# Performance work log

Hardware: AMD Instinct MI355X
Metric: run time of the kernel (lower is better)

## Reference

```python
import jax, jax.numpy as jnp
import numpy as np

EPS = 1e-8           # torch F.cosine_similarity eps
GLOBAL_COEFF = 0.5   # config.global_coeff


def setup_inputs() -> dict:
    key = jax.random.key(0)
    k1, k2, k3 = jax.random.split(key, 3)
    B, P, D = 8192, 1024, 2048
    return {
        "ppg": jax.random.normal(k1, (B, 1, D), dtype=jnp.float32),
        "keys": jax.random.normal(k2, (P, D), dtype=jnp.float32),
        "prompt": jax.random.normal(k3, (P, D), dtype=jnp.float32),
        "k": 5,
    }


def reference(ppg, keys, prompt, k):
    # ppg: [B,1,D], keys/prompt: [P,D]
    q = ppg[:, 0, :]                                   # [B,D]
    dot = jnp.einsum('bd,pd->bp', q, keys)             # [B,P]
    qn = jnp.linalg.norm(q, axis=-1, keepdims=True)    # [B,1]
    kn = jnp.linalg.norm(keys, axis=-1)[None, :]       # [1,P]
    cos = dot / jnp.maximum(qn * kn, EPS)
    score_ = 1.0 - cos                                 # [B,P]

    # top-k smallest distances
    neg_vals, idx = jax.lax.top_k(-score_, k)          # idx: [B,k]
    sel_score = -neg_vals                              # [B,k]

    # softmax over pool, global entropy (summed over batch AND pool, as in torch code)
    logp = jax.nn.log_softmax(score_, axis=-1)
    probs = jnp.exp(logp)
    entropy = -jnp.sum(probs * logp)

    # masked prompt aggregation == sum of the k selected prompts per batch element
    # (original builds a [B,P,D] mask; gather is the same math without the blowup)
    sel_prompts = prompt[idx]                          # [B,k,D]
    agg = sel_prompts.sum(axis=1)[:, None, :]          # [B,1,D]

    prompted = ppg + GLOBAL_COEFF * agg                # [B,1,D]
    # score.sum() in torch: (score_ * topk_mask).sum() == sel_score.sum()
    return prompted, sel_score.sum(), entropy
```

## Files before the change

### kernel.cpp

```cpp
#include <hip/hip_runtime.h>
#include <stdint.h>

#define NB 8192
#define NP 1024
#define ND 2048
#define KSEL 5

typedef unsigned short u16;
typedef unsigned int u32;
typedef unsigned long long u64;
typedef __attribute__((ext_vector_type(8))) short bf16x8;
typedef __attribute__((ext_vector_type(8))) u16 u16x8;
typedef __attribute__((ext_vector_type(4))) u16 u16x4;
typedef __attribute__((ext_vector_type(4))) float f32x4;

__device__ float g_knf[NP];
__device__ float g_qn[NB];
__device__ float g_psel[NB];
__device__ float g_pent[NB];
__device__ int   g_cidx[NB * 8];

__device__ __forceinline__ u16 f2bf_rne(float f) {
    u32 u = __float_as_uint(f);
    u = (u + 0x7fffu + ((u >> 16) & 1u)) >> 16;
    return (u16)u;
}


__global__ __launch_bounds__(256) void prep_q(const float* __restrict__ q,
                                              u16* __restrict__ qb) {
    const int r = blockIdx.x, t = threadIdx.x;
    const float* row = q + (size_t)r * ND;
    float4 a = *(const float4*)(row + t * 8);
    float4 b = *(const float4*)(row + t * 8 + 4);
    if (qb) {
        u16x8 v;
        v[0] = f2bf_rne(a.x); v[1] = f2bf_rne(a.y); v[2] = f2bf_rne(a.z); v[3] = f2bf_rne(a.w);
        v[4] = f2bf_rne(b.x); v[5] = f2bf_rne(b.y); v[6] = f2bf_rne(b.z); v[7] = f2bf_rne(b.w);
        *(u16x8*)(qb + (size_t)r * ND + t * 8) = v;
    }
    float ss = a.x*a.x + a.y*a.y + a.z*a.z + a.w*a.w
             + b.x*b.x + b.y*b.y + b.z*b.z + b.w*b.w;
    for (int off = 32; off; off >>= 1) ss += __shfl_xor(ss, off);
    __shared__ float red[4];
    if ((t & 63) == 0) red[t >> 6] = ss;
    __syncthreads();
    if (t == 0) g_qn[r] = sqrtf(red[0] + red[1] + red[2] + red[3]);
}

__global__ __launch_bounds__(256) void prep_k(const float* __restrict__ k,
                                              u16* __restrict__ kb) {
    const int r = blockIdx.x, t = threadIdx.x;
    const float* row = k + (size_t)r * ND;
    float4 a = *(const float4*)(row + t * 8);
    float4 b = *(const float4*)(row + t * 8 + 4);
    if (kb) {
        u16x8 v;
        v[0] = f2bf_rne(a.x); v[1] = f2bf_rne(a.y); v[2] = f2bf_rne(a.z); v[3] = f2bf_rne(a.w);
        v[4] = f2bf_rne(b.x); v[5] = f2bf_rne(b.y); v[6] = f2bf_rne(b.z); v[7] = f2bf_rne(b.w);
        *(u16x8*)(kb + (size_t)r * ND + t * 8) = v;
    }
    float ss = a.x*a.x + a.y*a.y + a.z*a.z + a.w*a.w
             + b.x*b.x + b.y*b.y + b.z*b.z + b.w*b.w;
    for (int off = 32; off; off >>= 1) ss += __shfl_xor(ss, off);
    __shared__ float red[4];
    if ((t & 63) == 0) red[t >> 6] = ss;
    __syncthreads();
    if (t == 0) g_knf[r] = sqrtf(red[0] + red[1] + red[2] + red[3]);
}


__global__ __launch_bounds__(256) void gemm_fast(const u16* __restrict__ A,
                                                 const u16* __restrict__ B,
                                                 float* __restrict__ C) {
    __shared__ u16 As[128 * 64];
    __shared__ u16 Bs[128 * 64];
    const int t = threadIdx.x, w = t >> 6, l = t & 63;
    const int bid = blockIdx.x;
    const int m0 = (bid >> 3) << 7, n0 = (bid & 7) << 7;
    const int wr = w >> 1, wc = w & 1;

    f32x4 acc[4][4];
#pragma unroll
    for (int m = 0; m < 4; m++)
#pragma unroll
        for (int n = 0; n < 4; n++) acc[m][n] = (f32x4){0.f, 0.f, 0.f, 0.f};

    const int rowi = l >> 3, col8 = l & 7;
    const u16* Abase = A + (size_t)(m0 + w * 8 + rowi) * ND + col8 * 8;
    const u16* Bbase = B + (size_t)(n0 + w * 8 + rowi) * ND + col8 * 8;

    for (int k0 = 0; k0 < ND; k0 += 64) {
#pragma unroll
        for (int i = 0; i < 4; i++) {
            __builtin_amdgcn_global_load_lds(
                (const __attribute__((address_space(1))) void*)(Abase + (size_t)(i * 32) * ND + k0),
                (__attribute__((address_space(3))) void*)(&As[(i * 4 + w) * 512]),
                16, 0, 0);
            __builtin_amdgcn_global_load_lds(
                (const __attribute__((address_space(1))) void*)(Bbase + (size_t)(i * 32) * ND + k0),
                (__attribute__((address_space(3))) void*)(&Bs[(i * 4 + w) * 512]),
                16, 0, 0);
        }
        __syncthreads();
#pragma unroll
        for (int kk = 0; kk < 64; kk += 32) {
            bf16x8 af[4], bfr[4];
#pragma unroll
            for (int m = 0; m < 4; m++)
                af[m] = *(const bf16x8*)&As[(wr * 64 + m * 16 + (l & 15)) * 64 + kk + (l >> 4) * 8];
#pragma unroll
            for (int n = 0; n < 4; n++)
                bfr[n] = *(const bf16x8*)&Bs[(wc * 64 + n * 16 + (l & 15)) * 64 + kk + (l >> 4) * 8];
#pragma unroll
            for (int m = 0; m < 4; m++)
#pragma unroll
                for (int n = 0; n < 4; n++)
                    acc[m][n] = __builtin_amdgcn_mfma_f32_16x16x32_bf16(af[m], bfr[n], acc[m][n], 0, 0, 0);
        }
        __syncthreads();
    }

    const int lc = l & 15, lr4 = (l >> 4) * 4;
#pragma unroll
    for (int m = 0; m < 4; m++) {
        int rbase = m0 + wr * 64 + m * 16 + lr4;
#pragma unroll
        for (int n = 0; n < 4; n++) {
            int col = n0 + wc * 64 + n * 16 + lc;
#pragma unroll
            for (int r = 0; r < 4; r++)
                C[(size_t)(rbase + r) * NP + col] = acc[m][n][r];
        }
    }
}


__global__ __launch_bounds__(256) void gemm_slow(const float* __restrict__ A,
                                                 const float* __restrict__ B,
                                                 float* __restrict__ C) {
    __shared__ u16 As[128 * 64];
    __shared__ u16 Bs[128 * 64];
    const int t = threadIdx.x, w = t >> 6, l = t & 63;
    const int bid = blockIdx.x;
    const int m0 = (bid >> 3) << 7, n0 = (bid & 7) << 7;
    const int wr = w >> 1, wc = w & 1;

    f32x4 acc[4][4];
#pragma unroll
    for (int m = 0; m < 4; m++)
#pragma unroll
        for (int n = 0; n < 4; n++) acc[m][n] = (f32x4){0.f, 0.f, 0.f, 0.f};

    const int arow = t >> 4;
    const int acol4 = t & 15;

    for (int k0 = 0; k0 < ND; k0 += 64) {
#pragma unroll
        for (int s = 0; s < 8; s++) {
            int row = s * 16 + arow;
            float4 va = *(const float4*)(A + (size_t)(m0 + row) * ND + k0 + acol4 * 4);
            u16x4 ba;
            ba[0] = f2bf_rne(va.x); ba[1] = f2bf_rne(va.y);
            ba[2] = f2bf_rne(va.z); ba[3] = f2bf_rne(va.w);
            *(u16x4*)&As[row * 64 + acol4 * 4] = ba;
            float4 vb = *(const float4*)(B + (size_t)(n0 + row) * ND + k0 + acol4 * 4);
            u16x4 bb;
            bb[0] = f2bf_rne(vb.x); bb[1] = f2bf_rne(vb.y);
            bb[2] = f2bf_rne(vb.z); bb[3] = f2bf_rne(vb.w);
            *(u16x4*)&Bs[row * 64 + acol4 * 4] = bb;
        }
        __syncthreads();
#pragma unroll
        for (int kk = 0; kk < 64; kk += 32) {
            bf16x8 af[4], bfr[4];
#pragma unroll
            for (int m = 0; m < 4; m++)
                af[m] = *(const bf16x8*)&As[(wr * 64 + m * 16 + (l & 15)) * 64 + kk + (l >> 4) * 8];
#pragma unroll
            for (int n = 0; n < 4; n++)
                bfr[n] = *(const bf16x8*)&Bs[(wc * 64 + n * 16 + (l & 15)) * 64 + kk + (l >> 4) * 8];
#pragma unroll
            for (int m = 0; m < 4; m++)
#pragma unroll
                for (int n = 0; n < 4; n++)
                    acc[m][n] = __builtin_amdgcn_mfma_f32_16x16x32_bf16(af[m], bfr[n], acc[m][n], 0, 0, 0);
        }
        __syncthreads();
    }

    const int lc = l & 15, lr4 = (l >> 4) * 4;
#pragma unroll
    for (int m = 0; m < 4; m++) {
        int rbase = m0 + wr * 64 + m * 16 + lr4;
#pragma unroll
        for (int n = 0; n < 4; n++) {
            int col = n0 + wc * 64 + n * 16 + lc;
#pragma unroll
            for (int r = 0; r < 4; r++)
                C[(size_t)(rbase + r) * NP + col] = acc[m][n][r];
        }
    }
}


__global__ __launch_bounds__(256) void rowstats(const float* __restrict__ C) {
    const int l = threadIdx.x & 63;
    const int r = blockIdx.x * 4 + (threadIdx.x >> 6);
    const float qn = g_qn[r];

    const float* crow = C + (size_t)r * NP;
    float s[16];
#pragma unroll
    for (int j = 0; j < 16; j++) {
        float dot = crow[j * 64 + l];
        float kn = g_knf[j * 64 + l];
        s[j] = 1.0f - dot / fmaxf(qn * kn, 1e-8f);
    }

    float mx = s[0];
#pragma unroll
    for (int j = 1; j < 16; j++) mx = fmaxf(mx, s[j]);
    for (int off = 32; off; off >>= 1) mx = fmaxf(mx, __shfl_xor(mx, off));
    float S0 = 0.f, S1 = 0.f;
#pragma unroll
    for (int j = 0; j < 16; j++) {
        float d = s[j] - mx;
        float e = __expf(d);
        S0 += e;
        S1 += d * e;
    }
    for (int off = 32; off; off >>= 1) {
        S0 += __shfl_xor(S0, off);
        S1 += __shfl_xor(S1, off);
    }

    unsigned used = 0;
    float ssum = 0.f;
    int ci[KSEL];
    for (int i = 0; i < KSEL; i++) {
        float bv = 3.0e38f;
        int bp = 0;
#pragma unroll
        for (int j = 0; j < 16; j++) {
            if (!((used >> j) & 1) && s[j] < bv) { bv = s[j]; bp = j * 64 + l; }
        }
        u64 u = ((u64)__float_as_uint(bv) << 32) | (u32)bp;
        for (int off = 32; off; off >>= 1) {
            u64 o = __shfl_xor(u, off);
            if (o < u) u = o;
        }
        int p = (int)(u & 0xffffffffu);
        ci[i] = p;
        ssum += __uint_as_float((u32)(u >> 32));
        if ((p & 63) == l) used |= 1u << (p >> 6);
    }
    if (l == 0) {
        g_pent[r] = logf(S0) - S1 / S0;
        g_psel[r] = ssum;
#pragma unroll
        for (int i = 0; i < KSEL; i++) g_cidx[r * 8 + i] = ci[i];
    }
}


__global__ __launch_bounds__(256) void gather_out(const float* __restrict__ ppg,
                                                  const float* __restrict__ prompt,
                                                  float* __restrict__ outp) {
    const int r = blockIdx.x, t = threadIdx.x;
    __shared__ int sel[KSEL];
    if (t < KSEL) sel[t] = g_cidx[r * 8 + t];
    __syncthreads();

    const float* prow = ppg + (size_t)r * ND + t * 8;
    float4 a = *(const float4*)prow;
    float4 b = *(const float4*)(prow + 4);
    float4 ax = {0, 0, 0, 0}, bx = {0, 0, 0, 0};
#pragma unroll
    for (int i = 0; i < KSEL; i++) {
        const float* pr = prompt + (size_t)sel[i] * ND + t * 8;
        float4 x = *(const float4*)pr;
        float4 y = *(const float4*)(pr + 4);
        ax.x += x.x; ax.y += x.y; ax.z += x.z; ax.w += x.w;
        bx.x += y.x; bx.y += y.y; bx.z += y.z; bx.w += y.w;
    }
    float4 oa = {a.x + 0.5f * ax.x, a.y + 0.5f * ax.y, a.z + 0.5f * ax.z, a.w + 0.5f * ax.w};
    float4 ob = {b.x + 0.5f * bx.x, b.y + 0.5f * bx.y, b.z + 0.5f * bx.z, b.w + 0.5f * bx.w};
    float* orow = outp + (size_t)r * ND + t * 8;
    *(float4*)orow = oa;
    *(float4*)(orow + 4) = ob;
}


__global__ __launch_bounds__(1024) void finalize_scal(float* __restrict__ outp) {
    const int t = threadIdx.x;
    float a = 0.f, b = 0.f;
#pragma unroll
    for (int i = 0; i < NB / 1024; i++) {
        a += g_psel[i * 1024 + t];
        b += g_pent[i * 1024 + t];
    }
    for (int off = 32; off; off >>= 1) {
        a += __shfl_xor(a, off);
        b += __shfl_xor(b, off);
    }
    __shared__ float ra[16], rb[16];
    if ((t & 63) == 0) { ra[t >> 6] = a; rb[t >> 6] = b; }
    __syncthreads();
    if (t == 0) {
        float sa = 0.f, sb = 0.f;
#pragma unroll
        for (int i = 0; i < 16; i++) { sa += ra[i]; sb += rb[i]; }
        outp[(size_t)NB * ND] = sa;
        outp[(size_t)NB * ND + 1] = sb;
    }
}

extern "C" void kernel_launch(void* const* d_in, const int* in_sizes, int n_in,
                              void* d_out, int out_size, void* d_ws, size_t ws_size,
                              hipStream_t stream) {
    const float* ppg    = (const float*)d_in[0];
    const float* keys   = (const float*)d_in[1];
    const float* prompt = (const float*)d_in[2];
    float* outp = (float*)d_out;

    float* C = (float*)d_out;

    const size_t QB_BYTES = (size_t)NB * ND * 2;
    const size_t KB_BYTES = (size_t)NP * ND * 2;
    bool fast = (d_ws != nullptr) && (ws_size >= QB_BYTES + KB_BYTES);
    u16* qb = fast ? (u16*)d_ws : nullptr;
    u16* kb = fast ? (u16*)((char*)d_ws + QB_BYTES) : nullptr;

    prep_q<<<NB, 256, 0, stream>>>(ppg, qb);
    prep_k<<<NP, 256, 0, stream>>>(keys, kb);
    if (fast) {
        gemm_fast<<<(NB / 128) * (NP / 128), 256, 0, stream>>>(qb, kb, C);
    } else {
        gemm_slow<<<(NB / 128) * (NP / 128), 256, 0, stream>>>(ppg, keys, C);
    }
    rowstats<<<NB / 4, 256, 0, stream>>>(C);
    gather_out<<<NB, 256, 0, stream>>>(ppg, prompt, outp);
    finalize_scal<<<1, 1024, 0, stream>>>(outp);
}
```

Measured before the change: 245.9 us.

## Fuse cosine epilogue into GEMM, store bf16 scores, merge rowstats with gather

The query and key prep kernels become one launch. The GEMM now runs 512 threads per block with a two-row-group load layout and an XCD-aware tile mapping, and its epilogue applies the cosine normalization and stores scores as bf16 into a global buffer. A single post kernel then computes the row softmax entropy, top-k and prompt gather-sum, which removes the fp32 score round-trip and the index buffer between kernels. Rounding scores to bf16 before top-k and entropy can reorder close candidates and shift the entropy.

```diff
diff --git a/kernel.cpp b/kernel.cpp
--- a/kernel.cpp
+++ b/kernel.cpp
@@ -18,26 +18,39 @@
 __device__ float g_qn[NB];
 __device__ float g_psel[NB];
 __device__ float g_pent[NB];
-__device__ int   g_cidx[NB * 8];
+__device__ u16   g_C[(size_t)NB * NP];
 
 __device__ __forceinline__ u16 f2bf_rne(float f) {
     u32 u = __float_as_uint(f);
     u = (u + 0x7fffu + ((u >> 16) & 1u)) >> 16;
     return (u16)u;
 }
-
-
-__global__ __launch_bounds__(256) void prep_q(const float* __restrict__ q,
-                                              u16* __restrict__ qb) {
-    const int r = blockIdx.x, t = threadIdx.x;
-    const float* row = q + (size_t)r * ND;
+__device__ __forceinline__ float bf2f(u16 v) {
+    return __uint_as_float(((u32)v) << 16);
+}
+
+
+__global__ __launch_bounds__(256) void prep(const float* __restrict__ q,
+                                            const float* __restrict__ k,
+                                            u16* __restrict__ qb,
+                                            u16* __restrict__ kb) {
+    const int rr = blockIdx.x, t = threadIdx.x;
+    const float* row;
+    u16* dst;
+    if (rr < NB) {
+        row = q + (size_t)rr * ND;
+        dst = qb ? qb + (size_t)rr * ND : nullptr;
+    } else {
+        row = k + (size_t)(rr - NB) * ND;
+        dst = kb ? kb + (size_t)(rr - NB) * ND : nullptr;
+    }
     float4 a = *(const float4*)(row + t * 8);
     float4 b = *(const float4*)(row + t * 8 + 4);
-    if (qb) {
+    if (dst) {
         u16x8 v;
         v[0] = f2bf_rne(a.x); v[1] = f2bf_rne(a.y); v[2] = f2bf_rne(a.z); v[3] = f2bf_rne(a.w);
         v[4] = f2bf_rne(b.x); v[5] = f2bf_rne(b.y); v[6] = f2bf_rne(b.z); v[7] = f2bf_rne(b.w);
-        *(u16x8*)(qb + (size_t)r * ND + t * 8) = v;
+        *(u16x8*)(dst + t * 8) = v;
     }
     float ss = a.x*a.x + a.y*a.y + a.z*a.z + a.w*a.w
              + b.x*b.x + b.y*b.y + b.z*b.z + b.w*b.w;
@@ -45,34 +58,86 @@
     __shared__ float red[4];
     if ((t & 63) == 0) red[t >> 6] = ss;
     __syncthreads();
-    if (t == 0) g_qn[r] = sqrtf(red[0] + red[1] + red[2] + red[3]);
-}
-
-__global__ __launch_bounds__(256) void prep_k(const float* __restrict__ k,
-                                              u16* __restrict__ kb) {
-    const int r = blockIdx.x, t = threadIdx.x;
-    const float* row = k + (size_t)r * ND;
-    float4 a = *(const float4*)(row + t * 8);
-    float4 b = *(const float4*)(row + t * 8 + 4);
-    if (kb) {
-        u16x8 v;
-        v[0] = f2bf_rne(a.x); v[1] = f2bf_rne(a.y); v[2] = f2bf_rne(a.z); v[3] = f2bf_rne(a.w);
-        v[4] = f2bf_rne(b.x); v[5] = f2bf_rne(b.y); v[6] = f2bf_rne(b.z); v[7] = f2bf_rne(b.w);
-        *(u16x8*)(kb + (size_t)r * ND + t * 8) = v;
-    }
-    float ss = a.x*a.x + a.y*a.y + a.z*a.z + a.w*a.w
-             + b.x*b.x + b.y*b.y + b.z*b.z + b.w*b.w;
-    for (int off = 32; off; off >>= 1) ss += __shfl_xor(ss, off);
-    __shared__ float red[4];
-    if ((t & 63) == 0) red[t >> 6] = ss;
-    __syncthreads();
-    if (t == 0) g_knf[r] = sqrtf(red[0] + red[1] + red[2] + red[3]);
-}
-
-
-__global__ __launch_bounds__(256) void gemm_fast(const u16* __restrict__ A,
-                                                 const u16* __restrict__ B,
-                                                 float* __restrict__ C) {
+    if (t == 0) {
+        float n = sqrtf(red[0] + red[1] + red[2] + red[3]);
+        if (rr < NB) g_qn[rr] = n; else g_knf[rr - NB] = n;
+    }
+}
+
+
+__global__ __launch_bounds__(512, 4) void gemm_fast(const u16* __restrict__ A,
+                                                    const u16* __restrict__ B) {
+    __shared__ u16 As[128 * 64];
+    __shared__ u16 Bs[128 * 64];
+    const int t = threadIdx.x, w = t >> 6, l = t & 63;
+    const int bid = blockIdx.x;
+    const int xcd = bid & 7, j = bid >> 3;
+    const int m0 = (xcd * 8 + (j & 7)) << 7;
+    const int n0 = (j >> 3) << 7;
+    const int wr = w >> 1, wc = w & 1;
+
+    f32x4 acc[2][4];
+#pragma unroll
+    for (int m = 0; m < 2; m++)
+#pragma unroll
+        for (int n = 0; n < 4; n++) acc[m][n] = (f32x4){0.f, 0.f, 0.f, 0.f};
+
+    const int rt = t >> 3, c8 = t & 7;
+    const u16* Abase = A + (size_t)(m0 + rt) * ND + c8 * 8;
+    const u16* Bbase = B + (size_t)(n0 + rt) * ND + c8 * 8;
+
+    for (int k0 = 0; k0 < ND; k0 += 64) {
+#pragma unroll
+        for (int i = 0; i < 2; i++) {
+            __builtin_amdgcn_global_load_lds(
+                (const __attribute__((address_space(1))) void*)(Abase + (size_t)(i * 64) * ND + k0),
+                (__attribute__((address_space(3))) void*)(&As[i * 4096 + w * 512]),
+                16, 0, 0);
+            __builtin_amdgcn_global_load_lds(
+                (const __attribute__((address_space(1))) void*)(Bbase + (size_t)(i * 64) * ND + k0),
+                (__attribute__((address_space(3))) void*)(&Bs[i * 4096 + w * 512]),
+                16, 0, 0);
+        }
+        __syncthreads();
+#pragma unroll
+        for (int kk = 0; kk < 64; kk += 32) {
+            bf16x8 af[2], bfr[4];
+#pragma unroll
+            for (int m = 0; m < 2; m++)
+                af[m] = *(const bf16x8*)&As[(wr * 32 + m * 16 + (l & 15)) * 64 + kk + (l >> 4) * 8];
+#pragma unroll
+            for (int n = 0; n < 4; n++)
+                bfr[n] = *(const bf16x8*)&Bs[(wc * 64 + n * 16 + (l & 15)) * 64 + kk + (l >> 4) * 8];
+#pragma unroll
+            for (int m = 0; m < 2; m++)
+#pragma unroll
+                for (int n = 0; n < 4; n++)
+                    acc[m][n] = __builtin_amdgcn_mfma_f32_16x16x32_bf16(af[m], bfr[n], acc[m][n], 0, 0, 0);
+        }
+        __syncthreads();
+    }
+
+    const int lc = l & 15, lr4 = (l >> 4) * 4;
+#pragma unroll
+    for (int m = 0; m < 2; m++) {
+        int rbase = m0 + wr * 32 + m * 16 + lr4;
+#pragma unroll
+        for (int n = 0; n < 4; n++) {
+            int col = n0 + wc * 64 + n * 16 + lc;
+            float kn = g_knf[col];
+#pragma unroll
+            for (int r = 0; r < 4; r++) {
+                int row = rbase + r;
+                float s = 1.0f - acc[m][n][r] / fmaxf(g_qn[row] * kn, 1e-8f);
+                g_C[(size_t)row * NP + col] = f2bf_rne(s);
+            }
+        }
+    }
+}
+
+
+__global__ __launch_bounds__(256) void gemm_slow(const float* __restrict__ A,
+                                                 const float* __restrict__ B) {
     __shared__ u16 As[128 * 64];
     __shared__ u16 Bs[128 * 64];
     const int t = threadIdx.x, w = t >> 6, l = t & 63;
@@ -86,74 +151,7 @@
 #pragma unroll
         for (int n = 0; n < 4; n++) acc[m][n] = (f32x4){0.f, 0.f, 0.f, 0.f};
 
-    const int rowi = l >> 3, col8 = l & 7;
-    const u16* Abase = A + (size_t)(m0 + w * 8 + rowi) * ND + col8 * 8;
-    const u16* Bbase = B + (size_t)(n0 + w * 8 + rowi) * ND + col8 * 8;
-
-    for (int k0 = 0; k0 < ND; k0 += 64) {
-#pragma unroll
-        for (int i = 0; i < 4; i++) {
-            __builtin_amdgcn_global_load_lds(
-                (const __attribute__((address_space(1))) void*)(Abase + (size_t)(i * 32) * ND + k0),
-                (__attribute__((address_space(3))) void*)(&As[(i * 4 + w) * 512]),
-                16, 0, 0);
-            __builtin_amdgcn_global_load_lds(
-                (const __attribute__((address_space(1))) void*)(Bbase + (size_t)(i * 32) * ND + k0),
-                (__attribute__((address_space(3))) void*)(&Bs[(i * 4 + w) * 512]),
-                16, 0, 0);
-        }
-        __syncthreads();
-#pragma unroll
-        for (int kk = 0; kk < 64; kk += 32) {
-            bf16x8 af[4], bfr[4];
-#pragma unroll
-            for (int m = 0; m < 4; m++)
-                af[m] = *(const bf16x8*)&As[(wr * 64 + m * 16 + (l & 15)) * 64 + kk + (l >> 4) * 8];
-#pragma unroll
-            for (int n = 0; n < 4; n++)
-                bfr[n] = *(const bf16x8*)&Bs[(wc * 64 + n * 16 + (l & 15)) * 64 + kk + (l >> 4) * 8];
-#pragma unroll
-            for (int m = 0; m < 4; m++)
-#pragma unroll
-                for (int n = 0; n < 4; n++)
-                    acc[m][n] = __builtin_amdgcn_mfma_f32_16x16x32_bf16(af[m], bfr[n], acc[m][n], 0, 0, 0);
-        }
-        __syncthreads();
-    }
-
-    const int lc = l & 15, lr4 = (l >> 4) * 4;
-#pragma unroll
-    for (int m = 0; m < 4; m++) {
-        int rbase = m0 + wr * 64 + m * 16 + lr4;
-#pragma unroll
-        for (int n = 0; n < 4; n++) {
-            int col = n0 + wc * 64 + n * 16 + lc;
-#pragma unroll
-            for (int r = 0; r < 4; r++)
-                C[(size_t)(rbase + r) * NP + col] = acc[m][n][r];
-        }
-    }
-}
-
-
-__global__ __launch_bounds__(256) void gemm_slow(const float* __restrict__ A,
-                                                 const float* __restrict__ B,
-                                                 float* __restrict__ C) {
-    __shared__ u16 As[128 * 64];
-    __shared__ u16 Bs[128 * 64];
-    const int t = threadIdx.x, w = t >> 6, l = t & 63;
-    const int bid = blockIdx.x;
-    const int m0 = (bid >> 3) << 7, n0 = (bid & 7) << 7;
-    const int wr = w >> 1, wc = w & 1;
-
-    f32x4 acc[4][4];
-#pragma unroll
-    for (int m = 0; m < 4; m++)
-#pragma unroll
-        for (int n = 0; n < 4; n++) acc[m][n] = (f32x4){0.f, 0.f, 0.f, 0.f};
-
-    const int arow = t >> 4;
-    const int acol4 = t & 15;
+    const int arow = t >> 4, acol4 = t & 15;
 
     for (int k0 = 0; k0 < ND; k0 += 64) {
 #pragma unroll
@@ -196,27 +194,28 @@
 #pragma unroll
         for (int n = 0; n < 4; n++) {
             int col = n0 + wc * 64 + n * 16 + lc;
-#pragma unroll
-            for (int r = 0; r < 4; r++)
-                C[(size_t)(rbase + r) * NP + col] = acc[m][n][r];
-        }
-    }
-}
-
-
-__global__ __launch_bounds__(256) void rowstats(const float* __restrict__ C) {
-    const int l = threadIdx.x & 63;
-    const int r = blockIdx.x * 4 + (threadIdx.x >> 6);
-    const float qn = g_qn[r];
-
-    const float* crow = C + (size_t)r * NP;
+            float kn = g_knf[col];
+#pragma unroll
+            for (int r = 0; r < 4; r++) {
+                int row = rbase + r;
+                float s = 1.0f - acc[m][n][r] / fmaxf(g_qn[row] * kn, 1e-8f);
+                g_C[(size_t)row * NP + col] = f2bf_rne(s);
+            }
+        }
+    }
+}
+
+
+__global__ __launch_bounds__(64) void post(const float* __restrict__ ppg,
+                                           const float* __restrict__ prompt,
+                                           float* __restrict__ outp) {
+    const int r = blockIdx.x, l = threadIdx.x;
+
+    u16x8 v0 = *(const u16x8*)&g_C[(size_t)r * NP + l * 16];
+    u16x8 v1 = *(const u16x8*)&g_C[(size_t)r * NP + l * 16 + 8];
     float s[16];
 #pragma unroll
-    for (int j = 0; j < 16; j++) {
-        float dot = crow[j * 64 + l];
-        float kn = g_knf[j * 64 + l];
-        s[j] = 1.0f - dot / fmaxf(qn * kn, 1e-8f);
-    }
+    for (int j = 0; j < 8; j++) { s[j] = bf2f(v0[j]); s[8 + j] = bf2f(v1[j]); }
 
     float mx = s[0];
 #pragma unroll
@@ -237,13 +236,13 @@
 
     unsigned used = 0;
     float ssum = 0.f;
-    int ci[KSEL];
+    int sel[KSEL];
     for (int i = 0; i < KSEL; i++) {
         float bv = 3.0e38f;
         int bp = 0;
 #pragma unroll
         for (int j = 0; j < 16; j++) {
-            if (!((used >> j) & 1) && s[j] < bv) { bv = s[j]; bp = j * 64 + l; }
+            if (!((used >> j) & 1) && s[j] < bv) { bv = s[j]; bp = l * 16 + j; }
         }
         u64 u = ((u64)__float_as_uint(bv) << 32) | (u32)bp;
         for (int off = 32; off; off >>= 1) {
@@ -251,44 +250,38 @@
             if (o < u) u = o;
         }
         int p = (int)(u & 0xffffffffu);
-        ci[i] = p;
+        sel[i] = p;
         ssum += __uint_as_float((u32)(u >> 32));
-        if ((p & 63) == l) used |= 1u << (p >> 6);
+        if ((p >> 4) == l) used |= 1u << (p & 15);
     }
     if (l == 0) {
         g_pent[r] = logf(S0) - S1 / S0;
         g_psel[r] = ssum;
-#pragma unroll
-        for (int i = 0; i < KSEL; i++) g_cidx[r * 8 + i] = ci[i];
-    }
-}
-
-
-__global__ __launch_bounds__(256) void gather_out(const float* __restrict__ ppg,
-                                                  const float* __restrict__ prompt,
-                                                  float* __restrict__ outp) {
-    const int r = blockIdx.x, t = threadIdx.x;
-    __shared__ int sel[KSEL];
-    if (t < KSEL) sel[t] = g_cidx[r * 8 + t];
-    __syncthreads();
-
-    const float* prow = ppg + (size_t)r * ND + t * 8;
-    float4 a = *(const float4*)prow;
-    float4 b = *(const float4*)(prow + 4);
-    float4 ax = {0, 0, 0, 0}, bx = {0, 0, 0, 0};
-#pragma unroll
-    for (int i = 0; i < KSEL; i++) {
-        const float* pr = prompt + (size_t)sel[i] * ND + t * 8;
-        float4 x = *(const float4*)pr;
-        float4 y = *(const float4*)(pr + 4);
-        ax.x += x.x; ax.y += x.y; ax.z += x.z; ax.w += x.w;
-        bx.x += y.x; bx.y += y.y; bx.z += y.z; bx.w += y.w;
-    }
-    float4 oa = {a.x + 0.5f * ax.x, a.y + 0.5f * ax.y, a.z + 0.5f * ax.z, a.w + 0.5f * ax.w};
-    float4 ob = {b.x + 0.5f * bx.x, b.y + 0.5f * bx.y, b.z + 0.5f * bx.z, b.w + 0.5f * bx.w};
-    float* orow = outp + (size_t)r * ND + t * 8;
-    *(float4*)orow = oa;
-    *(float4*)(orow + 4) = ob;
+    }
+
+    const float* prow = ppg + (size_t)r * ND;
+    float* orow = outp + (size_t)r * ND;
+    const float* p0 = prompt + (size_t)sel[0] * ND;
+    const float* p1 = prompt + (size_t)sel[1] * ND;
+    const float* p2 = prompt + (size_t)sel[2] * ND;
+    const float* p3 = prompt + (size_t)sel[3] * ND;
+    const float* p4 = prompt + (size_t)sel[4] * ND;
+#pragma unroll
+    for (int j = 0; j < 8; j++) {
+        int o = (j * 64 + l) * 4;
+        float4 a = *(const float4*)(prow + o);
+        float4 x0 = *(const float4*)(p0 + o);
+        float4 x1 = *(const float4*)(p1 + o);
+        float4 x2 = *(const float4*)(p2 + o);
+        float4 x3 = *(const float4*)(p3 + o);
+        float4 x4 = *(const float4*)(p4 + o);
+        float4 res;
+        res.x = a.x + 0.5f * (x0.x + x1.x + x2.x + x3.x + x4.x);
+        res.y = a.y + 0.5f * (x0.y + x1.y + x2.y + x3.y + x4.y);
+        res.z = a.z + 0.5f * (x0.z + x1.z + x2.z + x3.z + x4.z);
+        res.w = a.w + 0.5f * (x0.w + x1.w + x2.w + x3.w + x4.w);
+        *(float4*)(orow + o) = res;
+    }
 }
 
 
@@ -324,22 +317,18 @@
     const float* prompt = (const float*)d_in[2];
     float* outp = (float*)d_out;
 
-    float* C = (float*)d_out;
-
     const size_t QB_BYTES = (size_t)NB * ND * 2;
     const size_t KB_BYTES = (size_t)NP * ND * 2;
     bool fast = (d_ws != nullptr) && (ws_size >= QB_BYTES + KB_BYTES);
     u16* qb = fast ? (u16*)d_ws : nullptr;
     u16* kb = fast ? (u16*)((char*)d_ws + QB_BYTES) : nullptr;
 
-    prep_q<<<NB, 256, 0, stream>>>(ppg, qb);
-    prep_k<<<NP, 256, 0, stream>>>(keys, kb);
+    prep<<<NB + NP, 256, 0, stream>>>(ppg, keys, qb, kb);
     if (fast) {
-        gemm_fast<<<(NB / 128) * (NP / 128), 256, 0, stream>>>(qb, kb, C);
+        gemm_fast<<<512, 512, 0, stream>>>(qb, kb);
     } else {
-        gemm_slow<<<(NB / 128) * (NP / 128), 256, 0, stream>>>(ppg, keys, C);
-    }
-    rowstats<<<NB / 4, 256, 0, stream>>>(C);
-    gather_out<<<NB, 256, 0, stream>>>(ppg, prompt, outp);
+        gemm_slow<<<512, 256, 0, stream>>>(ppg, keys);
+    }
+    post<<<NB, 64, 0, stream>>>(ppg, prompt, outp);
     finalize_scal<<<1, 1024, 0, stream>>>(outp);
 }
```

Measured after the change: 235.3 us. 4.3% less time.
